# Kernel optimization log

Measured on AMD Instinct MI355X. Metric: run time of the kernel, lower is better.

The kernel has to match this reference:

```python
import jax, jax.numpy as jnp
import numpy as np

M, N, F = 512, 128, 512  # molecules, atoms per molecule, feature dim
HID, OUT = F // 4, 1


def setup_inputs() -> dict:
    key = jax.random.key(0)
    k1, k2, k3 = jax.random.split(key, 3)
    h = jax.random.normal(k1, (M, N, F), dtype=jnp.float32)
    W1 = jax.random.normal(k2, (F, HID), dtype=jnp.float32) * (1.0 / np.sqrt(F))
    b1 = jnp.zeros((HID,), dtype=jnp.float32)
    W2 = jax.random.normal(k3, (HID, OUT), dtype=jnp.float32) * (1.0 / np.sqrt(HID))
    b2 = jnp.zeros((OUT,), dtype=jnp.float32)
    return {"h": h, "W1": W1, "b1": b1, "W2": W2, "b2": b2}


def reference(h, W1, b1, W2, b2):
    # method == 'weighted_summation'
    # gate MLP: Linear -> ReLU -> Linear -> Sigmoid, per atom
    w = jax.nn.sigmoid(jax.nn.relu(h @ W1 + b1) @ W2 + b2)  # [M, N, OUT]
    # per-molecule weighted sum over atoms: mm(w_h.T, h) for each molecule,
    # concatenated along dim 0 -> [M*OUT, F] (OUT=1 -> [M, F])
    out = jnp.einsum('mno,mnf->mof', w, h)  # [M, OUT, F]
    return out.reshape(M * OUT, F)
```

## Files before the change

### kernel.cpp

```cpp
#include <hip/hip_runtime.h>
#include <hip/hip_bf16.h>


typedef unsigned short u16;
typedef unsigned int u32;
typedef __bf16 bf16x8 __attribute__((ext_vector_type(8)));
typedef float f32x4 __attribute__((ext_vector_type(4)));
typedef u32 u32x4 __attribute__((ext_vector_type(4)));

#define M_MOL 512
#define N_ATOM 128
#define F_DIM 512
#define HID_DIM 128

static __device__ __forceinline__ u16 f2bf(float x) {
  u32 u = __float_as_uint(x);
  u32 r = (u + 0x7fffu + ((u >> 16) & 1u)) >> 16;
  return (u16)r;
}
static __device__ __forceinline__ bf16x8 load8bf(const u16* p) {
  u32x4 v = *(const u32x4*)p;
  return __builtin_bit_cast(bf16x8, v);
}
static __device__ __forceinline__ bf16x8 pack8(u32x4 a, u32x4 b) {
  u32x4 r;
  r[0] = (a[0] >> 16) | (a[1] & 0xffff0000u);
  r[1] = (a[2] >> 16) | (a[3] & 0xffff0000u);
  r[2] = (b[0] >> 16) | (b[1] & 0xffff0000u);
  r[3] = (b[2] >> 16) | (b[3] & 0xffff0000u);
  return __builtin_bit_cast(bf16x8, r);
}

__global__ __launch_bounds__(256) void transpose_w1(const float* __restrict__ W1,
                                                    u16* __restrict__ W1T) {
  __shared__ float tile[64][65];
  const int k0 = blockIdx.x * 64;
  const int n0 = blockIdx.y * 64;
  const int t = threadIdx.x;
  #pragma unroll
  for (int i = 0; i < 16; ++i) {
    const int lin = i * 256 + t;
    const int lr = lin >> 6, lc = lin & 63;
    tile[lc][lr] = W1[(size_t)(k0 + lr) * HID_DIM + (n0 + lc)];
  }
  __syncthreads();
  #pragma unroll
  for (int i = 0; i < 16; ++i) {
    const int lin = i * 256 + t;
    const int wr = lin >> 6, wc = lin & 63;
    W1T[(size_t)(n0 + wr) * F_DIM + (k0 + wc)] = f2bf(tile[wr][wc]);
  }
}

__global__ __launch_bounds__(512, 4) void atom_pool_kernel(
    const float* __restrict__ h, const u16* __restrict__ W1T,
    const float* __restrict__ b1, const float* __restrict__ W2,
    const float* __restrict__ b2, float* __restrict__ out) {
  const int m = blockIdx.x;
  const int tid = threadIdx.x;
  const int wv = tid >> 6;
  const int lane = tid & 63;
  const int quad = lane >> 4;
  const int cl = lane & 15;

  __shared__ float w_s[N_ATOM];
  __shared__ float red[8][F_DIM];

  const float* hm = h + (size_t)m * N_ATOM * F_DIM;

  f32x4 acc[8];
  #pragma unroll
  for (int t = 0; t < 8; ++t) acc[t] = (f32x4){0.f, 0.f, 0.f, 0.f};

  const float* arow = hm + (size_t)(wv * 16 + cl) * F_DIM;
  const int kb = quad * 8;

  u32x4 a_lo = *(const u32x4*)(arow + kb);
  u32x4 a_hi = *(const u32x4*)(arow + kb + 4);
  #pragma unroll 2
  for (int ks = 0; ks < 16; ++ks) {
    const int k = ks * 32 + kb;
    bf16x8 afr = pack8(a_lo, a_hi);
    if (ks < 15) {
      a_lo = *(const u32x4*)(arow + k + 32);
      a_hi = *(const u32x4*)(arow + k + 36);
    }
    #pragma unroll
    for (int t = 0; t < 8; ++t) {
      bf16x8 bfr = load8bf(W1T + (size_t)(t * 16 + cl) * F_DIM + k);
      acc[t] = __builtin_amdgcn_mfma_f32_16x16x32_bf16(afr, bfr, acc[t], 0, 0, 0);
    }
  }

  float psum[4] = {0.f, 0.f, 0.f, 0.f};
  #pragma unroll
  for (int t = 0; t < 8; ++t) {
    const int hid = t * 16 + cl;
    const float b1v = b1[hid];
    const float w2v = W2[hid];
    #pragma unroll
    for (int r = 0; r < 4; ++r) {
      float tv = fmaxf(acc[t][r] + b1v, 0.f);
      psum[r] = fmaf(tv, w2v, psum[r]);
    }
  }
  #pragma unroll
  for (int off = 1; off < 16; off <<= 1)
    #pragma unroll
    for (int r = 0; r < 4; ++r)
      psum[r] += __shfl_xor(psum[r], off, 64);
  if (cl == 0) {
    const float b2v = b2[0];
    #pragma unroll
    for (int r = 0; r < 4; ++r) {
      const int atom = wv * 16 + quad * 4 + r;
      w_s[atom] = 1.f / (1.f + __expf(-(psum[r] + b2v)));
    }
  }
  __syncthreads();

  float facc[8] = {0.f, 0.f, 0.f, 0.f, 0.f, 0.f, 0.f, 0.f};
  const int f0 = lane * 8;
  const float* hrow = hm + (size_t)(wv * 16) * F_DIM + f0;
  #pragma unroll 4
  for (int i = 0; i < 16; ++i) {
    const float wn = w_s[wv * 16 + i];
    f32x4 h0 = *(const f32x4*)(hrow + (size_t)i * F_DIM);
    f32x4 h1 = *(const f32x4*)(hrow + (size_t)i * F_DIM + 4);
    #pragma unroll
    for (int j = 0; j < 4; ++j) {
      facc[j]     = fmaf(wn, h0[j], facc[j]);
      facc[j + 4] = fmaf(wn, h1[j], facc[j + 4]);
    }
  }
  #pragma unroll
  for (int j = 0; j < 8; ++j) red[wv][f0 + j] = facc[j];
  __syncthreads();

  {
    const int f = tid;
    float o = 0.f;
    #pragma unroll
    for (int k = 0; k < 8; ++k) o += red[k][f];
    out[(size_t)m * F_DIM + f] = o;
  }
}

extern "C" void kernel_launch(void* const* d_in, const int* in_sizes, int n_in,
                              void* d_out, int out_size, void* d_ws, size_t ws_size,
                              hipStream_t stream) {
  const float* h  = (const float*)d_in[0];
  const float* W1 = (const float*)d_in[1];
  const float* b1 = (const float*)d_in[2];
  const float* W2 = (const float*)d_in[3];
  const float* b2 = (const float*)d_in[4];
  float* out = (float*)d_out;
  u16* W1T = (u16*)d_ws;

  transpose_w1<<<dim3(8, 2), 256, 0, stream>>>(W1, W1T);
  atom_pool_kernel<<<M_MOL, 512, 0, stream>>>(h, W1T, b1, W2, b2, out);
}
```

Measured before the change: 249.5 us.

## Split molecules into two 64-atom blocks and stage W1T in LDS

```diff
diff --git a/kernel.cpp b/kernel.cpp
--- a/kernel.cpp
+++ b/kernel.cpp
@@ -6,21 +6,20 @@
 typedef unsigned int u32;
 typedef __bf16 bf16x8 __attribute__((ext_vector_type(8)));
 typedef float f32x4 __attribute__((ext_vector_type(4)));
+typedef float f32x2 __attribute__((ext_vector_type(2)));
 typedef u32 u32x4 __attribute__((ext_vector_type(4)));
 
 #define M_MOL 512
 #define N_ATOM 128
 #define F_DIM 512
 #define HID_DIM 128
+#define ABLK 64
+#define NBLK (M_MOL * 2)
 
 static __device__ __forceinline__ u16 f2bf(float x) {
   u32 u = __float_as_uint(x);
   u32 r = (u + 0x7fffu + ((u >> 16) & 1u)) >> 16;
   return (u16)r;
-}
-static __device__ __forceinline__ bf16x8 load8bf(const u16* p) {
-  u32x4 v = *(const u32x4*)p;
-  return __builtin_bit_cast(bf16x8, v);
 }
 static __device__ __forceinline__ bf16x8 pack8(u32x4 a, u32x4 b) {
   u32x4 r;
@@ -52,42 +51,60 @@
   }
 }
 
-__global__ __launch_bounds__(512, 4) void atom_pool_kernel(
+__global__ __launch_bounds__(256, 4) void pool_partial(
     const float* __restrict__ h, const u16* __restrict__ W1T,
     const float* __restrict__ b1, const float* __restrict__ W2,
-    const float* __restrict__ b2, float* __restrict__ out) {
-  const int m = blockIdx.x;
+    const float* __restrict__ b2, float* __restrict__ part) {
+  __shared__ union SM {
+    u16 bt[HID_DIM * 32];
+    float red[4][F_DIM];
+  } sm;
+  __shared__ float w_s[ABLK];
+
+  const int blk = blockIdx.x;
   const int tid = threadIdx.x;
   const int wv = tid >> 6;
   const int lane = tid & 63;
   const int quad = lane >> 4;
   const int cl = lane & 15;
 
-  __shared__ float w_s[N_ATOM];
-  __shared__ float red[8][F_DIM];
+  const float* hb = h + (size_t)blk * ABLK * F_DIM;
 
-  const float* hm = h + (size_t)m * N_ATOM * F_DIM;
+  const float* arow = hb + (size_t)(wv * 16 + cl) * F_DIM;
+  const int kb = quad * 8;
+
+  const int srow = tid >> 1;
+  const int scol = (tid & 1) * 16;
+  const u16* sg = W1T + (size_t)srow * F_DIM + scol;
+  u16* sl = sm.bt + srow * 32 + scol;
 
   f32x4 acc[8];
   #pragma unroll
   for (int t = 0; t < 8; ++t) acc[t] = (f32x4){0.f, 0.f, 0.f, 0.f};
 
-  const float* arow = hm + (size_t)(wv * 16 + cl) * F_DIM;
-  const int kb = quad * 8;
-
+  u32x4 st0 = *(const u32x4*)sg;
+  u32x4 st1 = *(const u32x4*)(sg + 8);
   u32x4 a_lo = *(const u32x4*)(arow + kb);
   u32x4 a_hi = *(const u32x4*)(arow + kb + 4);
+
   #pragma unroll 2
   for (int ks = 0; ks < 16; ++ks) {
-    const int k = ks * 32 + kb;
+    __syncthreads();
+    *(u32x4*)sl = st0;
+    *(u32x4*)(sl + 8) = st1;
+    __syncthreads();
+    if (ks < 15) {
+      st0 = *(const u32x4*)(sg + (ks + 1) * 32);
+      st1 = *(const u32x4*)(sg + (ks + 1) * 32 + 8);
+    }
     bf16x8 afr = pack8(a_lo, a_hi);
     if (ks < 15) {
-      a_lo = *(const u32x4*)(arow + k + 32);
-      a_hi = *(const u32x4*)(arow + k + 36);
+      a_lo = *(const u32x4*)(arow + (ks + 1) * 32 + kb);
+      a_hi = *(const u32x4*)(arow + (ks + 1) * 32 + kb + 4);
     }
     #pragma unroll
     for (int t = 0; t < 8; ++t) {
-      bf16x8 bfr = load8bf(W1T + (size_t)(t * 16 + cl) * F_DIM + k);
+      bf16x8 bfr = *(const bf16x8*)(sm.bt + (t * 16 + cl) * 32 + kb);
       acc[t] = __builtin_amdgcn_mfma_f32_16x16x32_bf16(afr, bfr, acc[t], 0, 0, 0);
     }
   }
@@ -112,16 +129,14 @@
   if (cl == 0) {
     const float b2v = b2[0];
     #pragma unroll
-    for (int r = 0; r < 4; ++r) {
-      const int atom = wv * 16 + quad * 4 + r;
-      w_s[atom] = 1.f / (1.f + __expf(-(psum[r] + b2v)));
-    }
+    for (int r = 0; r < 4; ++r)
+      w_s[wv * 16 + quad * 4 + r] = 1.f / (1.f + __expf(-(psum[r] + b2v)));
   }
   __syncthreads();
 
   float facc[8] = {0.f, 0.f, 0.f, 0.f, 0.f, 0.f, 0.f, 0.f};
   const int f0 = lane * 8;
-  const float* hrow = hm + (size_t)(wv * 16) * F_DIM + f0;
+  const float* hrow = hb + (size_t)(wv * 16) * F_DIM + f0;
   #pragma unroll 4
   for (int i = 0; i < 16; ++i) {
     const float wn = w_s[wv * 16 + i];
@@ -134,16 +149,28 @@
     }
   }
   #pragma unroll
-  for (int j = 0; j < 8; ++j) red[wv][f0 + j] = facc[j];
+  for (int j = 0; j < 8; ++j) sm.red[wv][f0 + j] = facc[j];
   __syncthreads();
 
   {
-    const int f = tid;
-    float o = 0.f;
-    #pragma unroll
-    for (int k = 0; k < 8; ++k) o += red[k][f];
-    out[(size_t)m * F_DIM + f] = o;
+    const int f = tid * 2;
+    f32x2 o;
+    o[0] = sm.red[0][f] + sm.red[1][f] + sm.red[2][f] + sm.red[3][f];
+    o[1] = sm.red[0][f + 1] + sm.red[1][f + 1] + sm.red[2][f + 1] + sm.red[3][f + 1];
+    *(f32x2*)(part + (size_t)blk * F_DIM + f) = o;
   }
+}
+
+__global__ __launch_bounds__(256) void reduce_out(const float* __restrict__ part,
+                                                  float* __restrict__ out) {
+  const int m = blockIdx.x;
+  const int f = threadIdx.x * 2;
+  f32x2 a = *(const f32x2*)(part + (size_t)(2 * m) * F_DIM + f);
+  f32x2 b = *(const f32x2*)(part + (size_t)(2 * m + 1) * F_DIM + f);
+  f32x2 o;
+  o[0] = a[0] + b[0];
+  o[1] = a[1] + b[1];
+  *(f32x2*)(out + (size_t)m * F_DIM + f) = o;
 }
 
 extern "C" void kernel_launch(void* const* d_in, const int* in_sizes, int n_in,
@@ -155,8 +182,11 @@
   const float* W2 = (const float*)d_in[3];
   const float* b2 = (const float*)d_in[4];
   float* out = (float*)d_out;
+
   u16* W1T = (u16*)d_ws;
+  float* part = (float*)((char*)d_ws + HID_DIM * F_DIM * sizeof(u16));
 
   transpose_w1<<<dim3(8, 2), 256, 0, stream>>>(W1, W1T);
-  atom_pool_kernel<<<M_MOL, 512, 0, stream>>>(h, W1T, b1, W2, b2, out);
+  pool_partial<<<NBLK, 256, 0, stream>>>(h, W1T, b1, W2, b2, part);
+  reduce_out<<<M_MOL, 256, 0, stream>>>(part, out);
 }
```

After: 223.6 us. -10.4%, faster.
